# Kernel optimization log

Measured on AMD Instinct MI355X. Metric: run time of the kernel, lower is better.

## Reference

```python
import jax, jax.numpy as jnp
import numpy as np

N_SRC, N_DST, DEG = 100000, 50000, 16
NODE_IN, EDGE_IN, HID = 128, 64, 64
E = N_DST * DEG


def sparsemax(z):
    # z: [..., K]; sparsemax along last axis (Martins & Astudillo)
    z = z - jnp.max(z, axis=-1, keepdims=True)
    zs = -jnp.sort(-z, axis=-1)  # descending sort
    k_range = jnp.arange(1, z.shape[-1] + 1, dtype=z.dtype)
    cs = jnp.cumsum(zs, axis=-1)
    is_gt = (1.0 + k_range * zs > cs).astype(z.dtype)
    k = jnp.max(is_gt * k_range, axis=-1, keepdims=True)
    tau = (jnp.sum(is_gt * zs, axis=-1, keepdims=True) - 1.0) / k
    return jnp.maximum(z - tau, 0.0)


def setup_inputs() -> dict:
    key = jax.random.key(0)
    ks = jax.random.split(key, 8)
    s = 0.02
    return {
        "node_features": jax.random.normal(ks[0], (N_SRC, NODE_IN), jnp.float32),
        "edge_features": jax.random.normal(ks[1], (E, EDGE_IN), jnp.float32),
        "src_idx": jax.random.randint(ks[2], (E,), 0, N_SRC, jnp.int32),
        "We": s * jax.random.normal(ks[3], (EDGE_IN, HID), jnp.float32),
        "be": jnp.zeros((HID,), jnp.float32),
        "Wa": s * jax.random.normal(ks[4], (EDGE_IN, HID), jnp.float32),
        "ba": jnp.zeros((HID,), jnp.float32),
        "wa": s * jax.random.normal(ks[5], (HID,), jnp.float32),
        "Wo": s * jax.random.normal(ks[6], (NODE_IN + HID, HID), jnp.float32),
        "bo": jnp.zeros((HID,), jnp.float32),
        "Wn": s * jax.random.normal(ks[7], (NODE_IN + HID, HID), jnp.float32),
        "bn": jnp.zeros((HID,), jnp.float32),
        "n_dst": N_DST,
        "deg": DEG,
    }


def reference(node_features, edge_features, src_idx, We, be, Wa, ba, wa, Wo, bo, Wn, bn, n_dst, deg):
    # dropout is identity in eval / p=0
    h_dst = node_features[:n_dst]                               # [n_dst, node_in]
    # message_func: per-edge transforms
    e_out = jax.nn.relu(edge_features @ We + be)                # [E, hid]
    a = jax.nn.leaky_relu((edge_features @ Wa + ba) @ wa)       # [E]
    h_src_e = node_features[src_idx]                            # gather [E, node_in]
    m = jax.nn.relu(jnp.concatenate([h_src_e, e_out], axis=-1) @ Wo + bo)  # [E, hid]
    # reduce_func: mailbox is [n_dst, deg, .] (fixed in-degree graph)
    a = a.reshape(n_dst, deg)
    m = m.reshape(n_dst, deg, -1)
    alpha = sparsemax(a)                                        # [n_dst, deg]
    h_neigh = jnp.einsum('nd,ndh->nh', alpha, m)                # [n_dst, hid]
    # node update
    return jax.nn.relu(jnp.concatenate([h_dst, h_neigh], axis=-1) @ Wn + bn)
```

## Files before the change

### kernel.cpp

```cpp
#include <hip/hip_runtime.h>


#define ND 50000

typedef __bf16 bf16x8 __attribute__((ext_vector_type(8)));
typedef float f32x4 __attribute__((ext_vector_type(4)));

__device__ __forceinline__ void sync_wave() {
  asm volatile("s_waitcnt lgkmcnt(0)" ::: "memory");
}

__device__ __forceinline__ unsigned short f2bf(float x) {
  unsigned u = __float_as_uint(x);
  u += 0x7fffu + ((u >> 16) & 1u);
  return (unsigned short)(u >> 16);
}

union FragU { bf16x8 v; unsigned short u[8]; };

__device__ __forceinline__ bf16x8 ld_cvt8(const float* __restrict__ p, float* fr) {
  float4 f0 = *reinterpret_cast<const float4*>(p);
  float4 f1 = *reinterpret_cast<const float4*>(p + 4);
  fr[0]=f0.x; fr[1]=f0.y; fr[2]=f0.z; fr[3]=f0.w;
  fr[4]=f1.x; fr[5]=f1.y; fr[6]=f1.z; fr[7]=f1.w;
  FragU fu;
  #pragma unroll
  for (int j = 0; j < 8; ++j) fu.u[j] = f2bf(fr[j]);
  return fu.v;
}

extern "C" __global__ void gteast_prep(const float* __restrict__ Wa,
                                       const float* __restrict__ ba,
                                       const float* __restrict__ wa,
                                       float* __restrict__ vc) {
  const int k = threadIdx.x;
  if (k < 64) {
    float s = 0.f;
    for (int h = 0; h < 64; ++h) s += Wa[k * 64 + h] * wa[h];
    vc[k] = s;
  }
  if (k == 0) {
    float c = 0.f;
    for (int h = 0; h < 64; ++h) c += ba[h] * wa[h];
    vc[64] = c;
  }
}

#define MFMA(a, b, c) __builtin_amdgcn_mfma_f32_16x16x32_bf16((a), (b), (c), 0, 0, 0)

extern "C" __global__ void __launch_bounds__(256, 2)
gteast_edge(const float* __restrict__ nf, const float* __restrict__ ef,
            const int* __restrict__ src_idx,
            const float* __restrict__ We, const float* __restrict__ be,
            const float* __restrict__ Wo, const float* __restrict__ bo,
            const float* __restrict__ vc,
            float* __restrict__ hn_out) {
  __shared__ unsigned short WeT[64 * 72];
  __shared__ unsigned short WoT[64 * 200];
  __shared__ unsigned short Elds[4][16 * 72];

  const int tid = threadIdx.x;
  for (int i = tid; i < 64 * 64; i += 256) {
    int k = i >> 6, n = i & 63;
    WeT[n * 72 + k] = f2bf(We[i]);
  }
  for (int i = tid; i < 192 * 64; i += 256) {
    int k = i >> 6, n = i & 63;
    WoT[n * 200 + k] = f2bf(Wo[i]);
  }
  __syncthreads();

  const int lane = tid & 63, w = tid >> 6;
  const int q = lane >> 4, t = lane & 15;

  bf16x8 WeF[2][4], WoF[6][4];
  #pragma unroll
  for (int nt = 0; nt < 4; ++nt) {
    #pragma unroll
    for (int kc = 0; kc < 2; ++kc)
      WeF[kc][nt] = *reinterpret_cast<const bf16x8*>(&WeT[(nt * 16 + t) * 72 + kc * 32 + q * 8]);
    #pragma unroll
    for (int kc = 0; kc < 6; ++kc)
      WoF[kc][nt] = *reinterpret_cast<const bf16x8*>(&WoT[(nt * 16 + t) * 200 + kc * 32 + q * 8]);
  }
  float vsl[16];
  #pragma unroll
  for (int kc = 0; kc < 2; ++kc)
    for (int j = 0; j < 8; ++j) vsl[kc * 8 + j] = vc[kc * 32 + q * 8 + j];
  const float cval = vc[64];
  float beL[4], boL[4];
  #pragma unroll
  for (int nt = 0; nt < 4; ++nt) { beL[nt] = be[nt * 16 + t]; boL[nt] = bo[nt * 16 + t]; }

  unsigned short* E = Elds[w];
  const int wid = blockIdx.x * 4 + w;

  for (int it = 0; it < 8; ++it) {
    const int n = wid + it * 6252;
    if (n >= ND) continue;
    const long e0 = (long)n * 16;

    bf16x8 efr[2];
    float fr[8];
    float ap = 0.f;
    #pragma unroll
    for (int kc = 0; kc < 2; ++kc) {
      efr[kc] = ld_cvt8(ef + (e0 + t) * 64 + kc * 32 + q * 8, fr);
      #pragma unroll
      for (int j = 0; j < 8; ++j) ap += fr[j] * vsl[kc * 8 + j];
    }
    ap += __shfl_xor(ap, 16);
    ap += __shfl_xor(ap, 32);
    float a = ap + cval;
    a = a > 0.f ? a : 0.01f * a;

    #pragma unroll
    for (int nt = 0; nt < 4; ++nt) {
      f32x4 c = {0.f, 0.f, 0.f, 0.f};
      c = MFMA(efr[0], WeF[0][nt], c);
      c = MFMA(efr[1], WeF[1][nt], c);
      #pragma unroll
      for (int r = 0; r < 4; ++r) {
        float vv = fmaxf(c[r] + beL[nt], 0.f);
        E[(4 * q + r) * 72 + nt * 16 + t] = f2bf(vv);
      }
    }
    sync_wave();

    const int s = src_idx[e0 + t];
    const float* hp = nf + (long)s * 128;
    bf16x8 af[6];
    #pragma unroll
    for (int kc = 0; kc < 4; ++kc) af[kc] = ld_cvt8(hp + kc * 32 + q * 8, fr);
    af[4] = *reinterpret_cast<const bf16x8*>(&E[t * 72 + q * 8]);
    af[5] = *reinterpret_cast<const bf16x8*>(&E[t * 72 + 32 + q * 8]);

    f32x4 accM[4];
    #pragma unroll
    for (int nt = 0; nt < 4; ++nt) {
      f32x4 c = {0.f, 0.f, 0.f, 0.f};
      #pragma unroll
      for (int kc = 0; kc < 6; ++kc) c = MFMA(af[kc], WoF[kc][nt], c);
      #pragma unroll
      for (int r = 0; r < 4; ++r) c[r] = fmaxf(c[r] + boL[nt], 0.f);
      accM[nt] = c;
    }
    sync_wave();

    float z = a;
    #pragma unroll
    for (int k = 2; k <= 16; k <<= 1) {
      #pragma unroll
      for (int j = k >> 1; j > 0; j >>= 1) {
        float o = __shfl_xor(z, j);
        const bool upper = (t & j) != 0;
        const bool desc = (t & k) == 0;
        z = (upper != desc) ? fmaxf(z, o) : fminf(z, o);
      }
    }
    float cs = z;
    #pragma unroll
    for (int off = 1; off < 16; off <<= 1) {
      float o = __shfl_up(cs, off, 16);
      cs += (t >= off) ? o : 0.f;
    }
    const bool gt = 1.f + (float)(t + 1) * z > cs;
    float kf = gt ? (float)(t + 1) : 0.f;
    float sv = gt ? z : 0.f;
    #pragma unroll
    for (int m = 1; m < 16; m <<= 1) {
      kf = fmaxf(kf, __shfl_xor(kf, m));
      sv += __shfl_xor(sv, m);
    }
    const float tau = (sv - 1.f) / kf;
    const float alpha = fmaxf(a - tau, 0.f);

    float al[4];
    #pragma unroll
    for (int r = 0; r < 4; ++r) al[r] = __shfl(alpha, 4 * q + r);
    float p[4];
    #pragma unroll
    for (int nt = 0; nt < 4; ++nt) {
      p[nt] = al[0] * accM[nt][0] + al[1] * accM[nt][1] +
              al[2] * accM[nt][2] + al[3] * accM[nt][3];
      p[nt] += __shfl_xor(p[nt], 16);
      p[nt] += __shfl_xor(p[nt], 32);
    }
    const float pown = (q == 0) ? p[0] : (q == 1) ? p[1] : (q == 2) ? p[2] : p[3];
    hn_out[(long)n * 64 + lane] = pown;
  }
}

extern "C" __global__ void __launch_bounds__(256, 2)
gteast_out(const float* __restrict__ nf, const float* __restrict__ Wn,
           const float* __restrict__ bn, float* __restrict__ out) {
  __shared__ unsigned short WnT[64 * 200];
  const int tid = threadIdx.x;
  for (int i = tid; i < 192 * 64; i += 256) {
    int k = i >> 6, nn = i & 63;
    WnT[nn * 200 + k] = f2bf(Wn[i]);
  }
  __syncthreads();

  const int lane = tid & 63, w = tid >> 6, q = lane >> 4, t = lane & 15;
  bf16x8 WF[6][4];
  #pragma unroll
  for (int nt = 0; nt < 4; ++nt)
    #pragma unroll
    for (int kc = 0; kc < 6; ++kc)
      WF[kc][nt] = *reinterpret_cast<const bf16x8*>(&WnT[(nt * 16 + t) * 200 + kc * 32 + q * 8]);
  float bnL[4];
  #pragma unroll
  for (int nt = 0; nt < 4; ++nt) bnL[nt] = bn[nt * 16 + t];

  const int wid = blockIdx.x * 4 + w;
  for (int it = 0; it < 2; ++it) {
    const int tile = wid + it * 1564;
    const int r0 = tile * 16;
    if (r0 >= ND) continue;

    float fr[8];
    bf16x8 af[6];
    const float* hp = nf + (long)(r0 + t) * 128;
    #pragma unroll
    for (int kc = 0; kc < 4; ++kc) af[kc] = ld_cvt8(hp + kc * 32 + q * 8, fr);
    const float* gp = out + (long)(r0 + t) * 64;
    #pragma unroll
    for (int kc = 0; kc < 2; ++kc) af[4 + kc] = ld_cvt8(gp + kc * 32 + q * 8, fr);

    #pragma unroll
    for (int nt = 0; nt < 4; ++nt) {
      f32x4 c = {0.f, 0.f, 0.f, 0.f};
      #pragma unroll
      for (int kc = 0; kc < 6; ++kc) c = MFMA(af[kc], WF[kc][nt], c);
      #pragma unroll
      for (int r = 0; r < 4; ++r)
        out[(long)(r0 + 4 * q + r) * 64 + nt * 16 + t] = fmaxf(c[r] + bnL[nt], 0.f);
    }
  }
}

extern "C" void kernel_launch(void* const* d_in, const int* in_sizes, int n_in,
                              void* d_out, int out_size, void* d_ws, size_t ws_size,
                              hipStream_t stream) {
  const float* nf = (const float*)d_in[0];
  const float* ef = (const float*)d_in[1];
  const int* si   = (const int*)d_in[2];
  const float* We = (const float*)d_in[3];
  const float* be = (const float*)d_in[4];
  const float* Wa = (const float*)d_in[5];
  const float* ba = (const float*)d_in[6];
  const float* wa = (const float*)d_in[7];
  const float* Wo = (const float*)d_in[8];
  const float* bo = (const float*)d_in[9];
  const float* Wn = (const float*)d_in[10];
  const float* bn = (const float*)d_in[11];
  float* out = (float*)d_out;
  float* vc = (float*)d_ws;

  gteast_prep<<<1, 64, 0, stream>>>(Wa, ba, wa, vc);
  gteast_edge<<<1563, 256, 0, stream>>>(nf, ef, si, We, be, Wo, bo, vc, out);
  gteast_out<<<391, 256, 0, stream>>>(nf, Wn, bn, out);
}
```

Before: 418.5 us.

## Switch to 32x32x16 MFMA tiles, fuse prep kernel, prefetch gather indices

Edge and output kernels move from 16x16x32 to 32x32x16 bf16 MFMA, so each wave now handles two destination nodes (32 edges) per iteration and B fragments are read from LDS instead of being held in registers. The Wa·wa precompute is folded into the edge kernel, which drops one launch. Src indices are prefetched one iteration ahead, loads are issued before conversion, and float-to-bf16 packing uses a cheaper perm-based round. Contiguous per-wave node assignment and a halved grid change the load balance, and the rounding is now round-half-up rather than round-to-even.

```diff
diff --git a/kernel.cpp b/kernel.cpp
--- a/kernel.cpp
+++ b/kernel.cpp
@@ -4,7 +4,7 @@
 #define ND 50000
 
 typedef __bf16 bf16x8 __attribute__((ext_vector_type(8)));
-typedef float f32x4 __attribute__((ext_vector_type(4)));
+typedef float f32x16 __attribute__((ext_vector_type(16)));
 
 __device__ __forceinline__ void sync_wave() {
   asm volatile("s_waitcnt lgkmcnt(0)" ::: "memory");
@@ -16,136 +16,151 @@
   return (unsigned short)(u >> 16);
 }
 
-union FragU { bf16x8 v; unsigned short u[8]; };
-
-__device__ __forceinline__ bf16x8 ld_cvt8(const float* __restrict__ p, float* fr) {
-  float4 f0 = *reinterpret_cast<const float4*>(p);
-  float4 f1 = *reinterpret_cast<const float4*>(p + 4);
-  fr[0]=f0.x; fr[1]=f0.y; fr[2]=f0.z; fr[3]=f0.w;
-  fr[4]=f1.x; fr[5]=f1.y; fr[6]=f1.z; fr[7]=f1.w;
-  FragU fu;
-  #pragma unroll
-  for (int j = 0; j < 8; ++j) fu.u[j] = f2bf(fr[j]);
-  return fu.v;
-}
-
-extern "C" __global__ void gteast_prep(const float* __restrict__ Wa,
-                                       const float* __restrict__ ba,
-                                       const float* __restrict__ wa,
-                                       float* __restrict__ vc) {
-  const int k = threadIdx.x;
-  if (k < 64) {
-    float s = 0.f;
-    for (int h = 0; h < 64; ++h) s += Wa[k * 64 + h] * wa[h];
-    vc[k] = s;
-  }
-  if (k == 0) {
-    float c = 0.f;
-    for (int h = 0; h < 64; ++h) c += ba[h] * wa[h];
-    vc[64] = c;
-  }
-}
-
-#define MFMA(a, b, c) __builtin_amdgcn_mfma_f32_16x16x32_bf16((a), (b), (c), 0, 0, 0)
+union Frag8 { bf16x8 v; unsigned u32[4]; };
+
+__device__ __forceinline__ bf16x8 pack44(float4 a, float4 b) {
+  Frag8 f;
+  f.u32[0] = __builtin_amdgcn_perm(__float_as_uint(a.y) + 0x8000u,
+                                   __float_as_uint(a.x) + 0x8000u, 0x07060302);
+  f.u32[1] = __builtin_amdgcn_perm(__float_as_uint(a.w) + 0x8000u,
+                                   __float_as_uint(a.z) + 0x8000u, 0x07060302);
+  f.u32[2] = __builtin_amdgcn_perm(__float_as_uint(b.y) + 0x8000u,
+                                   __float_as_uint(b.x) + 0x8000u, 0x07060302);
+  f.u32[3] = __builtin_amdgcn_perm(__float_as_uint(b.w) + 0x8000u,
+                                   __float_as_uint(b.z) + 0x8000u, 0x07060302);
+  return f.v;
+}
+
+#define MFMA32(a, b, c) __builtin_amdgcn_mfma_f32_32x32x16_bf16((a), (b), (c), 0, 0, 0)
+
+__device__ __forceinline__ f32x16 fzero16() {
+  f32x16 c;
+  #pragma unroll
+  for (int r = 0; r < 16; ++r) c[r] = 0.f;
+  return c;
+}
 
 extern "C" __global__ void __launch_bounds__(256, 2)
 gteast_edge(const float* __restrict__ nf, const float* __restrict__ ef,
-            const int* __restrict__ src_idx,
+            const int* __restrict__ src,
+            const float* __restrict__ Wa, const float* __restrict__ ba,
+            const float* __restrict__ wa,
             const float* __restrict__ We, const float* __restrict__ be,
             const float* __restrict__ Wo, const float* __restrict__ bo,
-            const float* __restrict__ vc,
             float* __restrict__ hn_out) {
+  __shared__ unsigned short WoT[64 * 200];
   __shared__ unsigned short WeT[64 * 72];
-  __shared__ unsigned short WoT[64 * 200];
-  __shared__ unsigned short Elds[4][16 * 72];
+  __shared__ unsigned short Et[4][32 * 72];
+  __shared__ float vls[65];
+  __shared__ float pr[260];
 
   const int tid = threadIdx.x;
-  for (int i = tid; i < 64 * 64; i += 256) {
-    int k = i >> 6, n = i & 63;
-    WeT[n * 72 + k] = f2bf(We[i]);
-  }
-  for (int i = tid; i < 192 * 64; i += 256) {
-    int k = i >> 6, n = i & 63;
-    WoT[n * 200 + k] = f2bf(Wo[i]);
+  for (int i = tid; i < 64 * 64; i += 256) WeT[(i & 63) * 72 + (i >> 6)] = f2bf(We[i]);
+  for (int i = tid; i < 192 * 64; i += 256) WoT[(i & 63) * 200 + (i >> 6)] = f2bf(Wo[i]);
+  {
+    const int k = tid >> 2, p = tid & 3;
+    float s = 0.f;
+    for (int h = 16 * p; h < 16 * p + 16; ++h) s += Wa[k * 64 + h] * wa[h];
+    pr[tid] = s;
+    if (tid < 4) {
+      float sc = 0.f;
+      for (int h = 16 * tid; h < 16 * tid + 16; ++h) sc += ba[h] * wa[h];
+      pr[256 + tid] = sc;
+    }
   }
   __syncthreads();
+  if (tid < 64) vls[tid] = pr[4 * tid] + pr[4 * tid + 1] + pr[4 * tid + 2] + pr[4 * tid + 3];
+  if (tid == 64) vls[64] = pr[256] + pr[257] + pr[258] + pr[259];
+  __syncthreads();
 
   const int lane = tid & 63, w = tid >> 6;
-  const int q = lane >> 4, t = lane & 15;
-
-  bf16x8 WeF[2][4], WoF[6][4];
-  #pragma unroll
-  for (int nt = 0; nt < 4; ++nt) {
-    #pragma unroll
-    for (int kc = 0; kc < 2; ++kc)
-      WeF[kc][nt] = *reinterpret_cast<const bf16x8*>(&WeT[(nt * 16 + t) * 72 + kc * 32 + q * 8]);
-    #pragma unroll
-    for (int kc = 0; kc < 6; ++kc)
-      WoF[kc][nt] = *reinterpret_cast<const bf16x8*>(&WoT[(nt * 16 + t) * 200 + kc * 32 + q * 8]);
-  }
-  float vsl[16];
-  #pragma unroll
-  for (int kc = 0; kc < 2; ++kc)
-    for (int j = 0; j < 8; ++j) vsl[kc * 8 + j] = vc[kc * 32 + q * 8 + j];
-  const float cval = vc[64];
-  float beL[4], boL[4];
-  #pragma unroll
-  for (int nt = 0; nt < 4; ++nt) { beL[nt] = be[nt * 16 + t]; boL[nt] = bo[nt * 16 + t]; }
-
-  unsigned short* E = Elds[w];
+  const int m = lane & 31, h8 = lane >> 5, t16 = lane & 15;
   const int wid = blockIdx.x * 4 + w;
-
+  if (wid >= 3125) return;
+
+  unsigned short* E = Et[w];
+  const float cval = vls[64];
+  float beL[2], boL[2];
+  beL[0] = be[m]; beL[1] = be[32 + m];
+  boL[0] = bo[m]; boL[1] = bo[32 + m];
+
+  int s_cur = src[wid * 256 + m];
+
+  #pragma unroll 2
   for (int it = 0; it < 8; ++it) {
-    const int n = wid + it * 6252;
-    if (n >= ND) continue;
-    const long e0 = (long)n * 16;
-
-    bf16x8 efr[2];
-    float fr[8];
+    const int n0 = wid * 16 + it * 2;
+    const long e0 = (long)wid * 256 + it * 32;
+
+    const int s_nxt = (it < 7) ? src[e0 + 32 + m] : 0;
+
+    const float* ep = ef + (e0 + m) * 64 + h8 * 8;
+    float4 er[8];
+    #pragma unroll
+    for (int kc = 0; kc < 4; ++kc) {
+      er[2 * kc] = *reinterpret_cast<const float4*>(ep + kc * 16);
+      er[2 * kc + 1] = *reinterpret_cast<const float4*>(ep + kc * 16 + 4);
+    }
+    const float* hp = nf + (long)s_cur * 128 + h8 * 8;
+    float4 nr[8];
+    #pragma unroll
+    for (int kc = 0; kc < 4; ++kc) {
+      nr[2 * kc] = *reinterpret_cast<const float4*>(hp + kc * 16);
+      nr[2 * kc + 1] = *reinterpret_cast<const float4*>(hp + kc * 16 + 4);
+    }
+
+    bf16x8 efF[4];
     float ap = 0.f;
     #pragma unroll
-    for (int kc = 0; kc < 2; ++kc) {
-      efr[kc] = ld_cvt8(ef + (e0 + t) * 64 + kc * 32 + q * 8, fr);
-      #pragma unroll
-      for (int j = 0; j < 8; ++j) ap += fr[j] * vsl[kc * 8 + j];
-    }
-    ap += __shfl_xor(ap, 16);
+    for (int kc = 0; kc < 4; ++kc) {
+      float4 a0 = er[2 * kc], a1 = er[2 * kc + 1];
+      float4 v0 = *reinterpret_cast<const float4*>(&vls[kc * 16 + h8 * 8]);
+      float4 v1 = *reinterpret_cast<const float4*>(&vls[kc * 16 + h8 * 8 + 4]);
+      ap += a0.x * v0.x + a0.y * v0.y + a0.z * v0.z + a0.w * v0.w;
+      ap += a1.x * v1.x + a1.y * v1.y + a1.z * v1.z + a1.w * v1.w;
+      efF[kc] = pack44(a0, a1);
+    }
     ap += __shfl_xor(ap, 32);
     float a = ap + cval;
     a = a > 0.f ? a : 0.01f * a;
 
     #pragma unroll
-    for (int nt = 0; nt < 4; ++nt) {
-      f32x4 c = {0.f, 0.f, 0.f, 0.f};
-      c = MFMA(efr[0], WeF[0][nt], c);
-      c = MFMA(efr[1], WeF[1][nt], c);
+    for (int nt = 0; nt < 2; ++nt) {
+      f32x16 c = fzero16();
       #pragma unroll
-      for (int r = 0; r < 4; ++r) {
-        float vv = fmaxf(c[r] + beL[nt], 0.f);
-        E[(4 * q + r) * 72 + nt * 16 + t] = f2bf(vv);
+      for (int kc = 0; kc < 4; ++kc)
+        c = MFMA32(efF[kc],
+                   *reinterpret_cast<const bf16x8*>(&WeT[(nt * 32 + m) * 72 + kc * 16 + h8 * 8]), c);
+      #pragma unroll
+      for (int r = 0; r < 16; ++r) {
+        const int row = (r & 3) + 8 * (r >> 2) + 4 * h8;
+        E[row * 72 + nt * 32 + m] = f2bf(fmaxf(c[r] + beL[nt], 0.f));
       }
     }
     sync_wave();
 
-    const int s = src_idx[e0 + t];
-    const float* hp = nf + (long)s * 128;
-    bf16x8 af[6];
-    #pragma unroll
-    for (int kc = 0; kc < 4; ++kc) af[kc] = ld_cvt8(hp + kc * 32 + q * 8, fr);
-    af[4] = *reinterpret_cast<const bf16x8*>(&E[t * 72 + q * 8]);
-    af[5] = *reinterpret_cast<const bf16x8*>(&E[t * 72 + 32 + q * 8]);
-
-    f32x4 accM[4];
-    #pragma unroll
-    for (int nt = 0; nt < 4; ++nt) {
-      f32x4 c = {0.f, 0.f, 0.f, 0.f};
-      #pragma unroll
-      for (int kc = 0; kc < 6; ++kc) c = MFMA(af[kc], WoF[kc][nt], c);
-      #pragma unroll
-      for (int r = 0; r < 4; ++r) c[r] = fmaxf(c[r] + boL[nt], 0.f);
-      accM[nt] = c;
+    float4 nr2[8];
+    #pragma unroll
+    for (int kc = 0; kc < 4; ++kc) {
+      nr2[2 * kc] = *reinterpret_cast<const float4*>(hp + 64 + kc * 16);
+      nr2[2 * kc + 1] = *reinterpret_cast<const float4*>(hp + 64 + kc * 16 + 4);
+    }
+
+    f32x16 cM0 = fzero16(), cM1 = fzero16();
+    #pragma unroll
+    for (int kc = 0; kc < 12; ++kc) {
+      bf16x8 af;
+      if (kc < 4) af = pack44(nr[2 * kc], nr[2 * kc + 1]);
+      else if (kc < 8) af = pack44(nr2[2 * (kc - 4)], nr2[2 * (kc - 4) + 1]);
+      else af = *reinterpret_cast<const bf16x8*>(&E[m * 72 + (kc - 8) * 16 + h8 * 8]);
+      cM0 = MFMA32(af, *reinterpret_cast<const bf16x8*>(&WoT[m * 200 + kc * 16 + h8 * 8]), cM0);
+      cM1 = MFMA32(af, *reinterpret_cast<const bf16x8*>(&WoT[(32 + m) * 200 + kc * 16 + h8 * 8]), cM1);
     }
     sync_wave();
+    #pragma unroll
+    for (int r = 0; r < 16; ++r) {
+      cM0[r] = fmaxf(cM0[r] + boL[0], 0.f);
+      cM1[r] = fmaxf(cM1[r] + boL[1], 0.f);
+    }
 
     float z = a;
     #pragma unroll
@@ -153,8 +168,8 @@
       #pragma unroll
       for (int j = k >> 1; j > 0; j >>= 1) {
         float o = __shfl_xor(z, j);
-        const bool upper = (t & j) != 0;
-        const bool desc = (t & k) == 0;
+        const bool upper = (t16 & j) != 0;
+        const bool desc = (t16 & k) == 0;
         z = (upper != desc) ? fmaxf(z, o) : fminf(z, o);
       }
     }
@@ -162,32 +177,37 @@
     #pragma unroll
     for (int off = 1; off < 16; off <<= 1) {
       float o = __shfl_up(cs, off, 16);
-      cs += (t >= off) ? o : 0.f;
-    }
-    const bool gt = 1.f + (float)(t + 1) * z > cs;
-    float kf = gt ? (float)(t + 1) : 0.f;
+      cs += (t16 >= off) ? o : 0.f;
+    }
+    const bool gt = 1.f + (float)(t16 + 1) * z > cs;
+    float kf = gt ? (float)(t16 + 1) : 0.f;
     float sv = gt ? z : 0.f;
     #pragma unroll
-    for (int m = 1; m < 16; m <<= 1) {
-      kf = fmaxf(kf, __shfl_xor(kf, m));
-      sv += __shfl_xor(sv, m);
+    for (int mm = 1; mm < 16; mm <<= 1) {
+      kf = fmaxf(kf, __shfl_xor(kf, mm));
+      sv += __shfl_xor(sv, mm);
     }
     const float tau = (sv - 1.f) / kf;
     const float alpha = fmaxf(a - tau, 0.f);
 
-    float al[4];
-    #pragma unroll
-    for (int r = 0; r < 4; ++r) al[r] = __shfl(alpha, 4 * q + r);
-    float p[4];
-    #pragma unroll
-    for (int nt = 0; nt < 4; ++nt) {
-      p[nt] = al[0] * accM[nt][0] + al[1] * accM[nt][1] +
-              al[2] * accM[nt][2] + al[3] * accM[nt][3];
-      p[nt] += __shfl_xor(p[nt], 16);
-      p[nt] += __shfl_xor(p[nt], 32);
-    }
-    const float pown = (q == 0) ? p[0] : (q == 1) ? p[1] : (q == 2) ? p[2] : p[3];
-    hn_out[(long)n * 64 + lane] = pown;
+    float al[16];
+    #pragma unroll
+    for (int r = 0; r < 16; ++r)
+      al[r] = __shfl(alpha, (r & 3) + 8 * (r >> 2) + 4 * h8);
+    float p00 = 0.f, p01 = 0.f, p10 = 0.f, p11 = 0.f;
+    #pragma unroll
+    for (int r = 0; r < 8; ++r) {
+      p00 += al[r] * cM0[r];      p01 += al[r] * cM1[r];
+      p10 += al[8 + r] * cM0[8 + r]; p11 += al[8 + r] * cM1[8 + r];
+    }
+    p00 += __shfl_xor(p00, 32); p01 += __shfl_xor(p01, 32);
+    p10 += __shfl_xor(p10, 32); p11 += __shfl_xor(p11, 32);
+    const float v0 = h8 ? p10 : p00;
+    const float v1 = h8 ? p11 : p01;
+    hn_out[(long)(n0 + h8) * 64 + m] = v0;
+    hn_out[(long)(n0 + h8) * 64 + 32 + m] = v1;
+
+    s_cur = s_nxt;
   }
 }
 
@@ -196,46 +216,57 @@
            const float* __restrict__ bn, float* __restrict__ out) {
   __shared__ unsigned short WnT[64 * 200];
   const int tid = threadIdx.x;
-  for (int i = tid; i < 192 * 64; i += 256) {
-    int k = i >> 6, nn = i & 63;
-    WnT[nn * 200 + k] = f2bf(Wn[i]);
-  }
+  for (int i = tid; i < 192 * 64; i += 256) WnT[(i & 63) * 200 + (i >> 6)] = f2bf(Wn[i]);
   __syncthreads();
 
-  const int lane = tid & 63, w = tid >> 6, q = lane >> 4, t = lane & 15;
-  bf16x8 WF[6][4];
-  #pragma unroll
-  for (int nt = 0; nt < 4; ++nt)
-    #pragma unroll
-    for (int kc = 0; kc < 6; ++kc)
-      WF[kc][nt] = *reinterpret_cast<const bf16x8*>(&WnT[(nt * 16 + t) * 200 + kc * 32 + q * 8]);
-  float bnL[4];
-  #pragma unroll
-  for (int nt = 0; nt < 4; ++nt) bnL[nt] = bn[nt * 16 + t];
-
-  const int wid = blockIdx.x * 4 + w;
-  for (int it = 0; it < 2; ++it) {
-    const int tile = wid + it * 1564;
-    const int r0 = tile * 16;
-    if (r0 >= ND) continue;
-
-    float fr[8];
-    bf16x8 af[6];
-    const float* hp = nf + (long)(r0 + t) * 128;
-    #pragma unroll
-    for (int kc = 0; kc < 4; ++kc) af[kc] = ld_cvt8(hp + kc * 32 + q * 8, fr);
-    const float* gp = out + (long)(r0 + t) * 64;
-    #pragma unroll
-    for (int kc = 0; kc < 2; ++kc) af[4 + kc] = ld_cvt8(gp + kc * 32 + q * 8, fr);
-
-    #pragma unroll
-    for (int nt = 0; nt < 4; ++nt) {
-      f32x4 c = {0.f, 0.f, 0.f, 0.f};
-      #pragma unroll
-      for (int kc = 0; kc < 6; ++kc) c = MFMA(af[kc], WF[kc][nt], c);
-      #pragma unroll
-      for (int r = 0; r < 4; ++r)
-        out[(long)(r0 + 4 * q + r) * 64 + nt * 16 + t] = fmaxf(c[r] + bnL[nt], 0.f);
+  const int lane = tid & 63, w = tid >> 6;
+  const int m = lane & 31, h8 = lane >> 5;
+  const int tile = blockIdx.x * 4 + w;
+  if (tile >= 1563) return;
+  const int r0 = tile * 32;
+
+  float bnL[2];
+  bnL[0] = bn[m]; bnL[1] = bn[32 + m];
+
+  const float* hp = nf + (long)(r0 + m) * 128 + h8 * 8;
+  const int hr = min(r0 + m, ND - 1);
+  const float* gp = out + (long)hr * 64 + h8 * 8;
+
+  float4 nr[8], nr2[8], gr[8];
+  #pragma unroll
+  for (int kc = 0; kc < 4; ++kc) {
+    nr[2 * kc] = *reinterpret_cast<const float4*>(hp + kc * 16);
+    nr[2 * kc + 1] = *reinterpret_cast<const float4*>(hp + kc * 16 + 4);
+  }
+  #pragma unroll
+  for (int kc = 0; kc < 4; ++kc) {
+    nr2[2 * kc] = *reinterpret_cast<const float4*>(hp + 64 + kc * 16);
+    nr2[2 * kc + 1] = *reinterpret_cast<const float4*>(hp + 64 + kc * 16 + 4);
+  }
+  #pragma unroll
+  for (int kc = 0; kc < 4; ++kc) {
+    gr[2 * kc] = *reinterpret_cast<const float4*>(gp + kc * 16);
+    gr[2 * kc + 1] = *reinterpret_cast<const float4*>(gp + kc * 16 + 4);
+  }
+
+  f32x16 c0 = fzero16(), c1 = fzero16();
+  #pragma unroll
+  for (int kc = 0; kc < 12; ++kc) {
+    bf16x8 af;
+    if (kc < 4) af = pack44(nr[2 * kc], nr[2 * kc + 1]);
+    else if (kc < 8) af = pack44(nr2[2 * (kc - 4)], nr2[2 * (kc - 4) + 1]);
+    else af = pack44(gr[2 * (kc - 8)], gr[2 * (kc - 8) + 1]);
+    c0 = MFMA32(af, *reinterpret_cast<const bf16x8*>(&WnT[m * 200 + kc * 16 + h8 * 8]), c0);
+    c1 = MFMA32(af, *reinterpret_cast<const bf16x8*>(&WnT[(32 + m) * 200 + kc * 16 + h8 * 8]), c1);
+  }
+
+  #pragma unroll
+  for (int r = 0; r < 16; ++r) {
+    const int row = (r & 3) + 8 * (r >> 2) + 4 * h8;
+    const int grow = r0 + row;
+    if (grow < ND) {
+      out[(long)grow * 64 + m] = fmaxf(c0[r] + bnL[0], 0.f);
+      out[(long)grow * 64 + 32 + m] = fmaxf(c1[r] + bnL[1], 0.f);
     }
   }
 }
@@ -256,9 +287,7 @@
   const float* Wn = (const float*)d_in[10];
   const float* bn = (const float*)d_in[11];
   float* out = (float*)d_out;
-  float* vc = (float*)d_ws;
-
-  gteast_prep<<<1, 64, 0, stream>>>(Wa, ba, wa, vc);
-  gteast_edge<<<1563, 256, 0, stream>>>(nf, ef, si, We, be, Wo, bo, vc, out);
+
+  gteast_edge<<<782, 256, 0, stream>>>(nf, ef, si, Wa, ba, wa, We, be, Wo, bo, out);
   gteast_out<<<391, 256, 0, stream>>>(nf, Wn, bn, out);
 }
```

Result: no change. 421.6 us (+0.7%).
